# Kernel tuning notes

Measured on AMD Instinct MI355X. Metric: run time of the kernel, lower is better.

The kernel has to match this reference:

```python
import jax, jax.numpy as jnp
import numpy as np

LN_EPS = 1e-5
RMS_EPS = 1.1920929e-07  # torch RMSNorm default eps=None -> finfo(fp32).eps

B, N, D = 16, 512, 512
H = 8
HD = D // H
U_EMBED = 6
DFF = 4 * D


def _layernorm(x, w, b):
    mu = jnp.mean(x, axis=-1, keepdims=True)
    var = jnp.mean((x - mu) ** 2, axis=-1, keepdims=True)
    return (x - mu) * jax.lax.rsqrt(var + LN_EPS) * w + b


def _rmsnorm(x, w):
    ms = jnp.mean(x * x, axis=-1, keepdims=True)
    return x * jax.lax.rsqrt(ms + RMS_EPS) * w


def setup_inputs() -> dict:
    key = jax.random.key(0)
    ks = jax.random.split(key, 16)
    s = 0.02
    return {
        "x": jax.random.normal(ks[0], (B, N, D), jnp.float32),
        "u": jax.random.normal(ks[1], (B, U_EMBED, N, N), jnp.float32),
        "ln1_w": jnp.ones((D,), jnp.float32),
        "ln1_b": jnp.zeros((D,), jnp.float32),
        "ln2_w": jnp.ones((D,), jnp.float32),
        "ln2_b": jnp.zeros((D,), jnp.float32),
        "wq": jax.random.normal(ks[2], (D, D), jnp.float32) * s,
        "wk": jax.random.normal(ks[3], (D, D), jnp.float32) * s,
        "wv": jax.random.normal(ks[4], (D, D), jnp.float32) * s,
        "wo": jax.random.normal(ks[5], (D, D), jnp.float32) * s,
        "bo": jnp.zeros((D,), jnp.float32),
        "u_w": jax.random.normal(ks[6], (H, U_EMBED), jnp.float32) * 0.1,  # 1x1 conv kernel
        "u_b": jnp.zeros((H,), jnp.float32),
        "rms_w": jnp.ones((D,), jnp.float32),
        "w1": jax.random.normal(ks[7], (DFF, D), jnp.float32) * s,
        "b1": jnp.zeros((DFF,), jnp.float32),
        "w2": jax.random.normal(ks[8], (D, DFF), jnp.float32) * s,
        "b2": jnp.zeros((D,), jnp.float32),
    }


def reference(x, u, ln1_w, ln1_b, ln2_w, ln2_b, wq, wk, wv, wo, bo,
              u_w, u_b, rms_w, w1, b1, w2, b2):
    x_res = x
    xn = _layernorm(x, ln1_w, ln1_b)

    # projections -> [B, H, N, HD]
    q = jnp.einsum("bnd,ed->bne", xn, wq).reshape(B, N, H, HD).transpose(0, 2, 1, 3)
    k = jnp.einsum("bnd,ed->bne", xn, wk).reshape(B, N, H, HD).transpose(0, 2, 1, 3)
    v = jnp.einsum("bnd,ed->bne", xn, wv).reshape(B, N, H, HD).transpose(0, 2, 1, 3)

    # NOTE: source divides by head_dim**-0.5 (i.e. multiplies by sqrt(head_dim))
    scores = jnp.einsum("bhnd,bhmd->bhnm", q, k) * jnp.sqrt(jnp.float32(HD))

    # 1x1 conv pairwise bias: [B, u_embed, N, N] -> [B, H, N, N]
    u_bias = jnp.einsum("bcnm,hc->bhnm", u, u_w) + u_b[None, :, None, None]
    scores = scores + u_bias

    attn_weights = jax.nn.softmax(scores, axis=-1)
    ctx = jnp.einsum("bhnm,bhmd->bhnd", attn_weights, v)
    ctx = ctx.transpose(0, 2, 1, 3).reshape(B, N, D)
    attn_out = jnp.einsum("bnd,ed->bne", ctx, wo) + bo

    h = _layernorm(attn_out, ln2_w, ln2_b) + x_res

    z = _rmsnorm(h, rms_w)
    z = jax.nn.silu(jnp.einsum("bnd,fd->bnf", z, w1) + b1)
    z = jnp.einsum("bnf,df->bnd", z, w2) + b2
    return (z + h, attn_weights)
```

## Files before the change

kernel.cpp:

```cpp
#include <hip/hip_runtime.h>
#include <math.h>

static constexpr int Bb  = 16;
static constexpr int Nn  = 512;
static constexpr int Dd  = 512;
static constexpr int Hh  = 8;
static constexpr int HDd = 64;
static constexpr int UEe = 6;
static constexpr int DFFf= 2048;

typedef __attribute__((ext_vector_type(8))) short short8v;
typedef __attribute__((ext_vector_type(4))) float f32x4;

__device__ __forceinline__ short f2bf(float f) {
  unsigned u = __float_as_uint(f);
  unsigned r = (u + 0x7fffu + ((u >> 16) & 1u)) >> 16;
  return (short)r;
}
__device__ __forceinline__ float bf2f(short h) {
  return __uint_as_float(((unsigned)(unsigned short)h) << 16);
}
__device__ __forceinline__ void split2(float v, short& hi, short& lo) {
  hi = f2bf(v);
  lo = f2bf(v - bf2f(hi));
}


__device__ __forceinline__ float2 block_sum2(float a, float b, float* sb) {
  #pragma unroll
  for (int o = 32; o; o >>= 1) { a += __shfl_down(a, o); b += __shfl_down(b, o); }
  const int lane = threadIdx.x & 63, wid = threadIdx.x >> 6;
  if (lane == 0) { sb[wid] = a; sb[4 + wid] = b; }
  __syncthreads();
  float ra = sb[0] + sb[1] + sb[2] + sb[3];
  float rb = sb[4] + sb[5] + sb[6] + sb[7];
  __syncthreads();
  return make_float2(ra, rb);
}

__device__ __forceinline__ float block_sum1(float a, float* sb) {
  #pragma unroll
  for (int o = 32; o; o >>= 1) a += __shfl_down(a, o);
  const int lane = threadIdx.x & 63, wid = threadIdx.x >> 6;
  if (lane == 0) sb[wid] = a;
  __syncthreads();
  float ra = sb[0] + sb[1] + sb[2] + sb[3];
  __syncthreads();
  return ra;
}


__global__ __launch_bounds__(256) void ln1_kernel(
    const float* __restrict__ x, const float* __restrict__ w,
    const float* __restrict__ b, short* __restrict__ oh, short* __restrict__ ol) {
  __shared__ float sb[8];
  const size_t row = blockIdx.x;
  const int t = threadIdx.x;
  const float* xr = x + row * Dd;
  float2 xv = *(const float2*)(xr + 2 * t);
  float2 r = block_sum2(xv.x + xv.y, xv.x * xv.x + xv.y * xv.y, sb);
  const float mu = r.x * (1.f / Dd);
  const float var = r.y * (1.f / Dd) - mu * mu;
  const float rstd = rsqrtf(var + 1e-5f);
  float2 wv = *(const float2*)(w + 2 * t);
  float2 bv = *(const float2*)(b + 2 * t);
  float v0 = (xv.x - mu) * rstd * wv.x + bv.x;
  float v1 = (xv.y - mu) * rstd * wv.y + bv.y;
  short2 h2, l2;
  split2(v0, h2.x, l2.x);
  split2(v1, h2.y, l2.y);
  *(short2*)(oh + row * Dd + 2 * t) = h2;
  *(short2*)(ol + row * Dd + 2 * t) = l2;
}


__global__ __launch_bounds__(256) void hz_kernel(
    const float* __restrict__ ao, const float* __restrict__ xres,
    const float* __restrict__ w, const float* __restrict__ b,
    const float* __restrict__ rw,
    float* __restrict__ h, short* __restrict__ zbf) {
  __shared__ float sb[8];
  const size_t row = blockIdx.x;
  const int t = threadIdx.x;
  float2 av = *(const float2*)(ao + row * Dd + 2 * t);
  float2 r = block_sum2(av.x + av.y, av.x * av.x + av.y * av.y, sb);
  const float mu = r.x * (1.f / Dd);
  const float var = r.y * (1.f / Dd) - mu * mu;
  const float rstd = rsqrtf(var + 1e-5f);
  float2 wv = *(const float2*)(w + 2 * t);
  float2 bv = *(const float2*)(b + 2 * t);
  float2 xv = *(const float2*)(xres + row * Dd + 2 * t);
  float2 hv;
  hv.x = (av.x - mu) * rstd * wv.x + bv.x + xv.x;
  hv.y = (av.y - mu) * rstd * wv.y + bv.y + xv.y;
  *(float2*)(h + row * Dd + 2 * t) = hv;
  float ms = block_sum1(hv.x * hv.x + hv.y * hv.y, sb) * (1.f / Dd);
  const float rr = rsqrtf(ms + 1.1920929e-07f);
  float2 rwv = *(const float2*)(rw + 2 * t);
  short2 zv;
  zv.x = f2bf(hv.x * rr * rwv.x);
  zv.y = f2bf(hv.y * rr * rwv.y);
  *(short2*)(zbf + row * Dd + 2 * t) = zv;
}


__global__ __launch_bounds__(256) void cvt_kernel(
    const float* __restrict__ in, short* __restrict__ out, int n4) {
  int i = blockIdx.x * 256 + threadIdx.x;
  if (i < n4) {
    float4 v = ((const float4*)in)[i];
    short4 o;
    o.x = f2bf(v.x); o.y = f2bf(v.y); o.z = f2bf(v.z); o.w = f2bf(v.w);
    ((short4*)out)[i] = o;
  }
}

__global__ __launch_bounds__(256) void cvt2_kernel(
    const float* __restrict__ in, short* __restrict__ hi,
    short* __restrict__ lo, int n4) {
  int i = blockIdx.x * 256 + threadIdx.x;
  if (i < n4) {
    float4 v = ((const float4*)in)[i];
    short4 h, l;
    split2(v.x, h.x, l.x); split2(v.y, h.y, l.y);
    split2(v.z, h.z, l.z); split2(v.w, h.w, l.w);
    ((short4*)hi)[i] = h;
    ((short4*)lo)[i] = l;
  }
}


__global__ __launch_bounds__(256) void vt_kernel(
    const short* __restrict__ v, short* __restrict__ vT) {
  __shared__ short Lt[64][72];
  const int z = blockIdx.y, b = z >> 3, hh = z & 7;
  const int n0 = blockIdx.x * 64;
  const int tid = threadIdx.x;
  #pragma unroll
  for (int it = 0; it < 2; ++it) {
    int id = tid + it * 256;
    int r = id >> 3, c8 = id & 7;
    *(short8v*)&Lt[r][c8 * 8] =
        *(const short8v*)(v + ((size_t)(b * Nn + n0 + r)) * Dd + hh * HDd + c8 * 8);
  }
  __syncthreads();
  #pragma unroll
  for (int it = 0; it < 2; ++it) {
    int id = tid + it * 256;
    int c = id >> 3, r8 = id & 7;
    short8v g;
    #pragma unroll
    for (int k = 0; k < 8; ++k) g[k] = Lt[r8 * 8 + k][c];
    *(short8v*)(vT + ((size_t)z * HDd + c) * Nn + n0 + r8 * 8) = g;
  }
}


__global__ __launch_bounds__(256) void mfma_qkv3_kernel(
    const short* __restrict__ Ah, const short* __restrict__ Al,
    const short* __restrict__ Wh, const short* __restrict__ Wl,
    short* __restrict__ qh_, short* __restrict__ ql_,
    short* __restrict__ kh_, short* __restrict__ kl_,
    short* __restrict__ vh_) {
  constexpr int MREP = 4, NREP = 2;
  __shared__ short Ash[128][40], Asl[128][40], Bsh[64][40], Bsl[64][40];
  const int tid = threadIdx.x;
  const int wave = tid >> 6, lane = tid & 63;
  const int wr = wave >> 1, wc = wave & 1;
  const int lrow = lane & 15, kblk = lane >> 4;
  const size_t bm = (size_t)blockIdx.y * 128, bn = (size_t)blockIdx.x * 64;
  f32x4 acc[MREP][NREP] = {};
  for (int k0 = 0; k0 < Dd; k0 += 32) {
    __syncthreads();
    #pragma unroll
    for (int it = 0; it < 2; ++it) {
      int id = tid + it * 256;
      int r = id >> 2, kq = id & 3;
      const size_t go = (bm + r) * Dd + k0 + kq * 8;
      *(short8v*)&Ash[r][kq * 8] = *(const short8v*)(Ah + go);
      *(short8v*)&Asl[r][kq * 8] = *(const short8v*)(Al + go);
    }
    {
      int r = tid >> 2, kq = tid & 3;
      const size_t go = (bn + r) * Dd + k0 + kq * 8;
      *(short8v*)&Bsh[r][kq * 8] = *(const short8v*)(Wh + go);
      *(short8v*)&Bsl[r][kq * 8] = *(const short8v*)(Wl + go);
    }
    __syncthreads();
    short8v afh[MREP], afl[MREP], bfh[NREP], bfl[NREP];
    #pragma unroll
    for (int i = 0; i < MREP; ++i) {
      afh[i] = *(const short8v*)&Ash[wr * 64 + i * 16 + lrow][kblk * 8];
      afl[i] = *(const short8v*)&Asl[wr * 64 + i * 16 + lrow][kblk * 8];
    }
    #pragma unroll
    for (int j = 0; j < NREP; ++j) {
      bfh[j] = *(const short8v*)&Bsh[wc * 32 + j * 16 + lrow][kblk * 8];
      bfl[j] = *(const short8v*)&Bsl[wc * 32 + j * 16 + lrow][kblk * 8];
    }
    #pragma unroll
    for (int i = 0; i < MREP; ++i)
      #pragma unroll
      for (int j = 0; j < NREP; ++j) {
        acc[i][j] = __builtin_amdgcn_mfma_f32_16x16x32_bf16(afh[i], bfh[j], acc[i][j], 0, 0, 0);
        acc[i][j] = __builtin_amdgcn_mfma_f32_16x16x32_bf16(afl[i], bfh[j], acc[i][j], 0, 0, 0);
        acc[i][j] = __builtin_amdgcn_mfma_f32_16x16x32_bf16(afh[i], bfl[j], acc[i][j], 0, 0, 0);
      }
  }
  const int seg = (int)(bn >> 9);
  short* dsth = seg == 0 ? qh_ : (seg == 1 ? kh_ : vh_);
  short* dstl = seg == 0 ? ql_ : kl_;
  #pragma unroll
  for (int i = 0; i < MREP; ++i) {
    #pragma unroll
    for (int j = 0; j < NREP; ++j) {
      const size_t gcol = (bn & 511) + wc * 32 + j * 16 + lrow;
      #pragma unroll
      for (int reg = 0; reg < 4; ++reg) {
        const size_t grow = bm + wr * 64 + i * 16 + kblk * 4 + reg;
        float vv = acc[i][j][reg];
        if (seg < 2) {
          short hh_, ll_;
          split2(vv, hh_, ll_);
          dsth[grow * Dd + gcol] = hh_;
          dstl[grow * Dd + gcol] = ll_;
        } else {
          dsth[grow * Dd + gcol] = f2bf(vv);
        }
      }
    }
  }
}


template <int EPI>
__global__ __launch_bounds__(256) void mfma_nt3_kernel(
    const short* __restrict__ Ah, const short* __restrict__ Al,
    const short* __restrict__ Wh, const short* __restrict__ Wl,
    void* __restrict__ C1, void* __restrict__ C2,
    const float* __restrict__ bias, int Nc, int K) {
  constexpr int BM = 128, BN = 64;
  constexpr int MREP = 4, NREP = 2;
  __shared__ short Ash[BM][40], Asl[BM][40], Bsh[BN][40], Bsl[BN][40];
  const int tid = threadIdx.x;
  const int wave = tid >> 6, lane = tid & 63;
  const int wr = wave >> 1, wc = wave & 1;
  const int lrow = lane & 15, kblk = lane >> 4;
  const size_t bm = (size_t)blockIdx.y * BM, bn = (size_t)blockIdx.x * BN;
  f32x4 acc[MREP][NREP] = {};
  for (int k0 = 0; k0 < K; k0 += 32) {
    __syncthreads();
    #pragma unroll
    for (int it = 0; it < 2; ++it) {
      int id = tid + it * 256;
      int r = id >> 2, kq = id & 3;
      const size_t go = (bm + r) * K + k0 + kq * 8;
      *(short8v*)&Ash[r][kq * 8] = *(const short8v*)(Ah + go);
      *(short8v*)&Asl[r][kq * 8] = *(const short8v*)(Al + go);
    }
    {
      int r = tid >> 2, kq = tid & 3;
      const size_t go = (bn + r) * K + k0 + kq * 8;
      *(short8v*)&Bsh[r][kq * 8] = *(const short8v*)(Wh + go);
      *(short8v*)&Bsl[r][kq * 8] = *(const short8v*)(Wl + go);
    }
    __syncthreads();
    short8v afh[MREP], afl[MREP], bfh[NREP], bfl[NREP];
    #pragma unroll
    for (int i = 0; i < MREP; ++i) {
      afh[i] = *(const short8v*)&Ash[wr * 64 + i * 16 + lrow][kblk * 8];
      afl[i] = *(const short8v*)&Asl[wr * 64 + i * 16 + lrow][kblk * 8];
    }
    #pragma unroll
    for (int j = 0; j < NREP; ++j) {
      bfh[j] = *(const short8v*)&Bsh[wc * 32 + j * 16 + lrow][kblk * 8];
      bfl[j] = *(const short8v*)&Bsl[wc * 32 + j * 16 + lrow][kblk * 8];
    }
    #pragma unroll
    for (int i = 0; i < MREP; ++i)
      #pragma unroll
      for (int j = 0; j < NREP; ++j) {
        acc[i][j] = __builtin_amdgcn_mfma_f32_16x16x32_bf16(afh[i], bfh[j], acc[i][j], 0, 0, 0);
        acc[i][j] = __builtin_amdgcn_mfma_f32_16x16x32_bf16(afl[i], bfh[j], acc[i][j], 0, 0, 0);
        acc[i][j] = __builtin_amdgcn_mfma_f32_16x16x32_bf16(afh[i], bfl[j], acc[i][j], 0, 0, 0);
      }
  }
  #pragma unroll
  for (int i = 0; i < MREP; ++i) {
    #pragma unroll
    for (int j = 0; j < NREP; ++j) {
      const size_t gcol = bn + wc * 32 + j * 16 + lrow;
      float bb = 0.f;
      if constexpr (EPI == 1) bb = bias[gcol];
      #pragma unroll
      for (int reg = 0; reg < 4; ++reg) {
        const size_t grow = bm + wr * 64 + i * 16 + kblk * 4 + reg;
        float vv = acc[i][j][reg] + bb;
        if constexpr (EPI == 0) {
          short hh_, ll_;
          split2(vv, hh_, ll_);
          ((short*)C1)[grow * Nc + gcol] = hh_;
          ((short*)C2)[grow * Nc + gcol] = ll_;
        } else if constexpr (EPI == 1) {
          ((float*)C1)[grow * Nc + gcol] = vv;
        } else {
          ((short*)C1)[grow * Nc + gcol] = f2bf(vv);
        }
      }
    }
  }
}


__global__ __launch_bounds__(256) void scores8_kernel(
    const short* __restrict__ qh, const short* __restrict__ ql,
    const short* __restrict__ kh, const short* __restrict__ kl,
    float* __restrict__ S, const float* __restrict__ u,
    const float* __restrict__ u_w, const float* __restrict__ u_b) {
  __shared__ __align__(16) char smem[36864];
  short (*Qsh)[72] = (short(*)[72])(smem + 0);
  short (*Qsl)[72] = (short(*)[72])(smem + 9216);
  short (*Ksh)[72] = (short(*)[72])(smem + 18432);
  short (*Ksl)[72] = (short(*)[72])(smem + 27648);
  float (*Sls)[68] = (float(*)[68])(smem);
  const int b = blockIdx.z;
  const int i0 = blockIdx.y * 64, j0 = blockIdx.x * 64;
  const int tid = threadIdx.x;
  const int wave = tid >> 6, lane = tid & 63;
  const int wr = wave >> 1, wc = wave & 1;
  const int lrow = lane & 15, kblk = lane >> 4;
  const int trow = tid >> 4;
  const int tcol = (tid & 15) * 4;
  const float* ub_ = u + (size_t)b * UEe * Nn * Nn;

  for (int h = 0; h < Hh; ++h) {
    __syncthreads();
    #pragma unroll
    for (int it = 0; it < 2; ++it) {
      int id = tid + it * 256;
      int r = id >> 3, kq = id & 7;
      const size_t gq = ((size_t)(b * Nn) + i0 + r) * Dd + h * HDd + kq * 8;
      const size_t gk = ((size_t)(b * Nn) + j0 + r) * Dd + h * HDd + kq * 8;
      *(short8v*)&Qsh[r][kq * 8] = *(const short8v*)(qh + gq);
      *(short8v*)&Qsl[r][kq * 8] = *(const short8v*)(ql + gq);
      *(short8v*)&Ksh[r][kq * 8] = *(const short8v*)(kh + gk);
      *(short8v*)&Ksl[r][kq * 8] = *(const short8v*)(kl + gk);
    }
    __syncthreads();
    f32x4 acc[2][2] = {};
    #pragma unroll
    for (int ks = 0; ks < 2; ++ks) {
      short8v afh[2], afl[2], bfh[2], bfl[2];
      #pragma unroll
      for (int i = 0; i < 2; ++i) {
        afh[i] = *(const short8v*)&Qsh[wr * 32 + i * 16 + lrow][ks * 32 + kblk * 8];
        afl[i] = *(const short8v*)&Qsl[wr * 32 + i * 16 + lrow][ks * 32 + kblk * 8];
      }
      #pragma unroll
      for (int j = 0; j < 2; ++j) {
        bfh[j] = *(const short8v*)&Ksh[wc * 32 + j * 16 + lrow][ks * 32 + kblk * 8];
        bfl[j] = *(const short8v*)&Ksl[wc * 32 + j * 16 + lrow][ks * 32 + kblk * 8];
      }
      #pragma unroll
      for (int i = 0; i < 2; ++i)
        #pragma unroll
        for (int j = 0; j < 2; ++j) {
          acc[i][j] = __builtin_amdgcn_mfma_f32_16x16x32_bf16(afh[i], bfh[j], acc[i][j], 0, 0, 0);
          acc[i][j] = __builtin_amdgcn_mfma_f32_16x16x32_bf16(afl[i], bfh[j], acc[i][j], 0, 0, 0);
          acc[i][j] = __builtin_amdgcn_mfma_f32_16x16x32_bf16(afh[i], bfl[j], acc[i][j], 0, 0, 0);
        }
    }
    __syncthreads();
    #pragma unroll
    for (int i = 0; i < 2; ++i)
      #pragma unroll
      for (int j = 0; j < 2; ++j)
        #pragma unroll
        for (int reg = 0; reg < 4; ++reg)
          Sls[wr * 32 + i * 16 + kblk * 4 + reg][wc * 32 + j * 16 + lrow] =
              8.f * acc[i][j][reg];
    __syncthreads();
    float uw[UEe];
    #pragma unroll
    for (int c = 0; c < UEe; ++c) uw[c] = u_w[h * UEe + c];
    const float ubh = u_b[h];
    float* Sp = S + ((size_t)(b * Hh + h)) * Nn * Nn;
    #pragma unroll
    for (int p = 0; p < 4; ++p) {
      const size_t goff = (size_t)(i0 + p * 16 + trow) * Nn + j0 + tcol;
      float4 v = *(const float4*)&Sls[p * 16 + trow][tcol];
      v.x += ubh; v.y += ubh; v.z += ubh; v.w += ubh;
      #pragma unroll
      for (int c = 0; c < UEe; ++c) {
        float4 uv = *(const float4*)(ub_ + (size_t)c * Nn * Nn + goff);
        v.x = fmaf(uw[c], uv.x, v.x);
        v.y = fmaf(uw[c], uv.y, v.y);
        v.z = fmaf(uw[c], uv.z, v.z);
        v.w = fmaf(uw[c], uv.w, v.w);
      }
      *(float4*)(Sp + goff) = v;
    }
  }
}


__global__ __launch_bounds__(256) void smctx_kernel(
    float* __restrict__ P, const short* __restrict__ vT,
    short* __restrict__ ctxh, short* __restrict__ ctxl) {
  __shared__ short Ps[32][520];
  __shared__ short Bs[64][136];
  const int z = blockIdx.y, b = z >> 3, hh = z & 7;
  const int row0 = blockIdx.x * 32;
  const int tid = threadIdx.x;
  const int lr = tid >> 3, sub = tid & 7;
  float* Sp = P + (size_t)z * Nn * Nn + (size_t)(row0 + lr) * Nn + sub * 64;
  float4 s[16];
  #pragma unroll
  for (int q = 0; q < 16; ++q) s[q] = *(const float4*)(Sp + q * 4);
  float m = -1e30f;
  #pragma unroll
  for (int q = 0; q < 16; ++q)
    m = fmaxf(m, fmaxf(fmaxf(s[q].x, s[q].y), fmaxf(s[q].z, s[q].w)));
  m = fmaxf(m, __shfl_xor(m, 1));
  m = fmaxf(m, __shfl_xor(m, 2));
  m = fmaxf(m, __shfl_xor(m, 4));
  float sum = 0.f;
  #pragma unroll
  for (int q = 0; q < 16; ++q) {
    s[q].x = __expf(s[q].x - m); s[q].y = __expf(s[q].y - m);
    s[q].z = __expf(s[q].z - m); s[q].w = __expf(s[q].w - m);
    sum += (s[q].x + s[q].y) + (s[q].z + s[q].w);
  }
  sum += __shfl_xor(sum, 1);
  sum += __shfl_xor(sum, 2);
  sum += __shfl_xor(sum, 4);
  const float rr = 1.f / sum;
  #pragma unroll
  for (int q = 0; q < 16; ++q) {
    s[q].x *= rr; s[q].y *= rr; s[q].z *= rr; s[q].w *= rr;
    *(float4*)(Sp + q * 4) = s[q];
  }
  #pragma unroll
  for (int q = 0; q < 8; ++q) {
    float4 a = s[2 * q], c = s[2 * q + 1];
    short8v pk;
    pk[0] = f2bf(a.x); pk[1] = f2bf(a.y); pk[2] = f2bf(a.z); pk[3] = f2bf(a.w);
    pk[4] = f2bf(c.x); pk[5] = f2bf(c.y); pk[6] = f2bf(c.z); pk[7] = f2bf(c.w);
    *(short8v*)&Ps[lr][sub * 64 + q * 8] = pk;
  }
  const int wave = tid >> 6, lane = tid & 63;
  const int wr = wave >> 1, wc = wave & 1;
  const int lrow = lane & 15, kblk = lane >> 4;
  f32x4 acc0 = {}, acc1 = {};
  for (int kc = 0; kc < 4; ++kc) {
    __syncthreads();
    #pragma unroll
    for (int it = 0; it < 4; ++it) {
      int id = tid + it * 256;
      int rrow = id >> 4, k8 = id & 15;
      *(short8v*)&Bs[rrow][k8 * 8] =
          *(const short8v*)(vT + ((size_t)z * HDd + rrow) * Nn + kc * 128 + k8 * 8);
    }
    __syncthreads();
    #pragma unroll
    for (int ks = 0; ks < 4; ++ks) {
      short8v af = *(const short8v*)&Ps[wr * 16 + lrow][kc * 128 + ks * 32 + kblk * 8];
      short8v b0 = *(const short8v*)&Bs[wc * 32 + lrow][ks * 32 + kblk * 8];
      short8v b1 = *(const short8v*)&Bs[wc * 32 + 16 + lrow][ks * 32 + kblk * 8];
      acc0 = __builtin_amdgcn_mfma_f32_16x16x32_bf16(af, b0, acc0, 0, 0, 0);
      acc1 = __builtin_amdgcn_mfma_f32_16x16x32_bf16(af, b1, acc1, 0, 0, 0);
    }
  }
  const size_t outbase =
      ((size_t)(b * Nn + row0 + wr * 16 + kblk * 4)) * Dd + hh * HDd + wc * 32 + lrow;
  #pragma unroll
  for (int reg = 0; reg < 4; ++reg) {
    short h0, l0, h1, l1;
    split2(acc0[reg], h0, l0);
    split2(acc1[reg], h1, l1);
    ctxh[outbase + (size_t)reg * Dd] = h0;
    ctxl[outbase + (size_t)reg * Dd] = l0;
    ctxh[outbase + (size_t)reg * Dd + 16] = h1;
    ctxl[outbase + (size_t)reg * Dd + 16] = l1;
  }
}


template <int BM, int BN, int EPI>
__global__ __launch_bounds__(256) void mfma_nt_kernel(
    const short* __restrict__ Ag, const short* __restrict__ Wg,
    void* __restrict__ Cv, const float* __restrict__ bias,
    const float* __restrict__ res, int Nc, int K) {
  constexpr int MREP = BM / 32, NREP = BN / 32;
  __shared__ short As[BM][72];
  __shared__ short Bs[BN][72];
  const int tid = threadIdx.x;
  const int wave = tid >> 6, lane = tid & 63;
  const int wr = wave >> 1, wc = wave & 1;
  const int lrow = lane & 15, kblk = lane >> 4;
  const size_t bm = (size_t)blockIdx.y * BM, bn = (size_t)blockIdx.x * BN;
  f32x4 acc[MREP][NREP] = {};
  for (int k0 = 0; k0 < K; k0 += 32) {
    __syncthreads();
    #pragma unroll
    for (int it = 0; it < BM / 64; ++it) {
      int id = tid + it * 256;
      int r = id >> 2, kq = id & 3;
      *(short8v*)&As[r][kq * 8] = *(const short8v*)(Ag + (bm + r) * K + k0 + kq * 8);
    }
    #pragma unroll
    for (int it = 0; it < BN / 64; ++it) {
      int id = tid + it * 256;
      int r = id >> 2, kq = id & 3;
      *(short8v*)&Bs[r][kq * 8] = *(const short8v*)(Wg + (bn + r) * K + k0 + kq * 8);
    }
    __syncthreads();
    short8v af[MREP], bf[NREP];
    #pragma unroll
    for (int i = 0; i < MREP; ++i)
      af[i] = *(const short8v*)&As[wr * (BM / 2) + i * 16 + lrow][kblk * 8];
    #pragma unroll
    for (int j = 0; j < NREP; ++j)
      bf[j] = *(const short8v*)&Bs[wc * (BN / 2) + j * 16 + lrow][kblk * 8];
    #pragma unroll
    for (int i = 0; i < MREP; ++i)
      #pragma unroll
      for (int j = 0; j < NREP; ++j)
        acc[i][j] = __builtin_amdgcn_mfma_f32_16x16x32_bf16(af[i], bf[j], acc[i][j], 0, 0, 0);
  }
  #pragma unroll
  for (int i = 0; i < MREP; ++i) {
    #pragma unroll
    for (int j = 0; j < NREP; ++j) {
      const size_t gcol = bn + wc * (BN / 2) + j * 16 + lrow;
      const float bb = bias[gcol];
      #pragma unroll
      for (int reg = 0; reg < 4; ++reg) {
        const size_t grow = bm + wr * (BM / 2) + i * 16 + kblk * 4 + reg;
        float vv = acc[i][j][reg] + bb;
        if constexpr (EPI == 0) {
          vv = vv / (1.f + __expf(-vv));
          ((short*)Cv)[grow * Nc + gcol] = f2bf(vv);
        } else {
          ((float*)Cv)[grow * Nc + gcol] = vv + res[grow * Nc + gcol];
        }
      }
    }
  }
}


extern "C" void kernel_launch(void* const* d_in, const int* in_sizes, int n_in,
                              void* d_out, int out_size, void* d_ws, size_t ws_size,
                              hipStream_t stream) {
  const float* x     = (const float*)d_in[0];
  const float* u     = (const float*)d_in[1];
  const float* ln1_w = (const float*)d_in[2];
  const float* ln1_b = (const float*)d_in[3];
  const float* ln2_w = (const float*)d_in[4];
  const float* ln2_b = (const float*)d_in[5];
  const float* wq    = (const float*)d_in[6];
  const float* wk    = (const float*)d_in[7];
  const float* wv    = (const float*)d_in[8];
  const float* wo    = (const float*)d_in[9];
  const float* bo    = (const float*)d_in[10];
  const float* u_w   = (const float*)d_in[11];
  const float* u_b   = (const float*)d_in[12];
  const float* rms_w = (const float*)d_in[13];
  const float* w1    = (const float*)d_in[14];
  const float* b1    = (const float*)d_in[15];
  const float* w2    = (const float*)d_in[16];
  const float* b2    = (const float*)d_in[17];

  float* out   = (float*)d_out;
  float* attnW = out + (size_t)Bb * Nn * Dd;

  const size_t SB = (size_t)Bb * Nn * Dd * 2;
  char* wsb = (char*)d_ws;
  short* xnh  = (short*)(wsb + 0 * SB);
  short* xnl  = (short*)(wsb + 1 * SB);
  short* qh   = (short*)(wsb + 2 * SB);
  short* ql   = (short*)(wsb + 3 * SB);
  short* kh   = (short*)(wsb + 4 * SB);
  short* kl   = (short*)(wsb + 5 * SB);
  short* vh   = (short*)(wsb + 6 * SB);
  short* vTh  = (short*)(wsb + 0 * SB);
  short* ctxh = (short*)(wsb + 1 * SB);
  short* ctxl = (short*)(wsb + 6 * SB);
  float* aout = (float*)(wsb + 2 * SB);
  float* hbuf = (float*)(wsb + 5 * SB);
  short* zbf  = (short*)(wsb + 0 * SB);
  short* h1bf = (short*)(wsb + 1 * SB);
  const size_t WTBYTES = 8 * (size_t)Dd * Dd * 2 + 2 * (size_t)DFFf * Dd * 2;
  const size_t wt = (ws_size - WTBYTES) & ~(size_t)255;
  short* wAh = (short*)(wsb + wt);
  short* wAl = wAh + 3 * (size_t)Dd * Dd;
  short* woh = wAl + 3 * (size_t)Dd * Dd;
  short* wol = woh + (size_t)Dd * Dd;
  short* w1h = wol + (size_t)Dd * Dd;
  short* w2h = w1h + (size_t)DFFf * Dd;

  const int MR = Bb * Nn;

  cvt2_kernel<<<256, 256, 0, stream>>>(wq, wAh, wAl, Dd * Dd / 4);
  cvt2_kernel<<<256, 256, 0, stream>>>(wk, wAh + (size_t)Dd * Dd, wAl + (size_t)Dd * Dd, Dd * Dd / 4);
  cvt2_kernel<<<256, 256, 0, stream>>>(wv, wAh + 2 * (size_t)Dd * Dd, wAl + 2 * (size_t)Dd * Dd, Dd * Dd / 4);
  cvt2_kernel<<<256, 256, 0, stream>>>(wo, woh, wol, Dd * Dd / 4);
  cvt_kernel<<<1024, 256, 0, stream>>>(w1, w1h, DFFf * Dd / 4);
  cvt_kernel<<<1024, 256, 0, stream>>>(w2, w2h, DFFf * Dd / 4);

  ln1_kernel<<<MR, 256, 0, stream>>>(x, ln1_w, ln1_b, xnh, xnl);

  dim3 gQKV(3 * Dd / 64, MR / 128);
  mfma_qkv3_kernel<<<gQKV,256,0,stream>>>(xnh, xnl, wAh, wAl, qh, ql, kh, kl, vh);

  dim3 gVt(Nn / 64, Bb * Hh);
  vt_kernel<<<gVt, 256, 0, stream>>>(vh, vTh);

  dim3 gSc(Nn / 64, Nn / 64, Bb);
  scores8_kernel<<<gSc, 256, 0, stream>>>(qh, ql, kh, kl, attnW, u, u_w, u_b);

  dim3 gSm(Nn / 32, Bb * Hh);
  smctx_kernel<<<gSm, 256, 0, stream>>>(attnW, vTh, ctxh, ctxl);

  dim3 gProj(Dd / 64, MR / 128);
  mfma_nt3_kernel<1><<<gProj,256,0,stream>>>(ctxh, ctxl, woh, wol, aout, nullptr, bo, Dd, Dd);

  hz_kernel<<<MR, 256, 0, stream>>>(aout, x, ln2_w, ln2_b, rms_w, hbuf, zbf);

  dim3 gF1(DFFf / 128, MR / 128);
  mfma_nt_kernel<128,128,0><<<gF1,256,0,stream>>>(
      zbf, w1h, h1bf, b1, nullptr, DFFf, Dd);
  dim3 gF2(Dd / 128, MR / 64);
  mfma_nt_kernel<64,128,1><<<gF2,256,0,stream>>>(
      h1bf, w2h, out, b2, hbuf, Dd, DFFf);
}
```

Measured before the change: 346.2 us.

## Fuse scores, pairwise bias, softmax and context into one attention kernel

Merges the scores kernel (QK^T plus 1x1-conv bias) and the softmax+PV kernel into a single kernel per (batch, head, 32-row block). Scores for a row block stay in registers, so the fp32 score matrix is written once as the final attention weights instead of being written, read back and rewritten. In exchange, the u bias tensor is now read once per head instead of once per batch across all heads, K is reloaded per 32-row block, and shared memory per block grows.

```diff
diff --git a/kernel.cpp b/kernel.cpp
--- a/kernel.cpp
+++ b/kernel.cpp
@@ -312,83 +312,78 @@
 }
 
 
-__global__ __launch_bounds__(256) void scores8_kernel(
+__global__ __launch_bounds__(256) void fattn_kernel(
     const short* __restrict__ qh, const short* __restrict__ ql,
     const short* __restrict__ kh, const short* __restrict__ kl,
-    float* __restrict__ S, const float* __restrict__ u,
-    const float* __restrict__ u_w, const float* __restrict__ u_b) {
-  __shared__ __align__(16) char smem[36864];
+    const short* __restrict__ vT, float* __restrict__ P,
+    const float* __restrict__ u, const float* __restrict__ u_w,
+    const float* __restrict__ u_b,
+    short* __restrict__ ctxh, short* __restrict__ ctxl) {
+  __shared__ __align__(16) char smem[50688];
   short (*Qsh)[72] = (short(*)[72])(smem + 0);
-  short (*Qsl)[72] = (short(*)[72])(smem + 9216);
-  short (*Ksh)[72] = (short(*)[72])(smem + 18432);
-  short (*Ksl)[72] = (short(*)[72])(smem + 27648);
-  float (*Sls)[68] = (float(*)[68])(smem);
-  const int b = blockIdx.z;
-  const int i0 = blockIdx.y * 64, j0 = blockIdx.x * 64;
+  short (*Qsl)[72] = (short(*)[72])(smem + 4608);
+  short (*Ksh)[72] = (short(*)[72])(smem + 9216);
+  short (*Ksl)[72] = (short(*)[72])(smem + 18432);
+  float (*Sls)[68] = (float(*)[68])(smem + 27648);
+  short (*Ps)[520] = (short(*)[520])(smem + 0);
+  short (*Bs)[136] = (short(*)[136])(smem + 33280);
+  const int z = blockIdx.y, b = z >> 3, h = z & 7;
+  const int row0 = blockIdx.x * 32;
   const int tid = threadIdx.x;
+  const int lr = tid >> 3, sub = tid & 7;
   const int wave = tid >> 6, lane = tid & 63;
   const int wr = wave >> 1, wc = wave & 1;
   const int lrow = lane & 15, kblk = lane >> 4;
-  const int trow = tid >> 4;
-  const int tcol = (tid & 15) * 4;
+
+  {
+    const size_t gq = ((size_t)(b * Nn) + row0 + lr) * Dd + h * HDd + sub * 8;
+    *(short8v*)&Qsh[lr][sub * 8] = *(const short8v*)(qh + gq);
+    *(short8v*)&Qsl[lr][sub * 8] = *(const short8v*)(ql + gq);
+  }
+  float uw[UEe];
+  #pragma unroll
+  for (int c = 0; c < UEe; ++c) uw[c] = u_w[h * UEe + c];
+  const float ubh = u_b[h];
   const float* ub_ = u + (size_t)b * UEe * Nn * Nn;
 
-  for (int h = 0; h < Hh; ++h) {
+  float4 s[16];
+  #pragma unroll
+  for (int jt = 0; jt < 8; ++jt) {
     __syncthreads();
     #pragma unroll
     for (int it = 0; it < 2; ++it) {
       int id = tid + it * 256;
       int r = id >> 3, kq = id & 7;
-      const size_t gq = ((size_t)(b * Nn) + i0 + r) * Dd + h * HDd + kq * 8;
-      const size_t gk = ((size_t)(b * Nn) + j0 + r) * Dd + h * HDd + kq * 8;
-      *(short8v*)&Qsh[r][kq * 8] = *(const short8v*)(qh + gq);
-      *(short8v*)&Qsl[r][kq * 8] = *(const short8v*)(ql + gq);
+      const size_t gk = ((size_t)(b * Nn) + jt * 64 + r) * Dd + h * HDd + kq * 8;
       *(short8v*)&Ksh[r][kq * 8] = *(const short8v*)(kh + gk);
       *(short8v*)&Ksl[r][kq * 8] = *(const short8v*)(kl + gk);
     }
     __syncthreads();
-    f32x4 acc[2][2] = {};
+    f32x4 acc[2] = {};
     #pragma unroll
     for (int ks = 0; ks < 2; ++ks) {
-      short8v afh[2], afl[2], bfh[2], bfl[2];
-      #pragma unroll
-      for (int i = 0; i < 2; ++i) {
-        afh[i] = *(const short8v*)&Qsh[wr * 32 + i * 16 + lrow][ks * 32 + kblk * 8];
-        afl[i] = *(const short8v*)&Qsl[wr * 32 + i * 16 + lrow][ks * 32 + kblk * 8];
+      short8v afh = *(const short8v*)&Qsh[wr * 16 + lrow][ks * 32 + kblk * 8];
+      short8v afl = *(const short8v*)&Qsl[wr * 16 + lrow][ks * 32 + kblk * 8];
+      #pragma unroll
+      for (int j = 0; j < 2; ++j) {
+        short8v bfh = *(const short8v*)&Ksh[wc * 32 + j * 16 + lrow][ks * 32 + kblk * 8];
+        short8v bfl = *(const short8v*)&Ksl[wc * 32 + j * 16 + lrow][ks * 32 + kblk * 8];
+        acc[j] = __builtin_amdgcn_mfma_f32_16x16x32_bf16(afh, bfh, acc[j], 0, 0, 0);
+        acc[j] = __builtin_amdgcn_mfma_f32_16x16x32_bf16(afl, bfh, acc[j], 0, 0, 0);
+        acc[j] = __builtin_amdgcn_mfma_f32_16x16x32_bf16(afh, bfl, acc[j], 0, 0, 0);
       }
-      #pragma unroll
-      for (int j = 0; j < 2; ++j) {
-        bfh[j] = *(const short8v*)&Ksh[wc * 32 + j * 16 + lrow][ks * 32 + kblk * 8];
-        bfl[j] = *(const short8v*)&Ksl[wc * 32 + j * 16 + lrow][ks * 32 + kblk * 8];
-      }
-      #pragma unroll
-      for (int i = 0; i < 2; ++i)
-        #pragma unroll
-        for (int j = 0; j < 2; ++j) {
-          acc[i][j] = __builtin_amdgcn_mfma_f32_16x16x32_bf16(afh[i], bfh[j], acc[i][j], 0, 0, 0);
-          acc[i][j] = __builtin_amdgcn_mfma_f32_16x16x32_bf16(afl[i], bfh[j], acc[i][j], 0, 0, 0);
-          acc[i][j] = __builtin_amdgcn_mfma_f32_16x16x32_bf16(afh[i], bfl[j], acc[i][j], 0, 0, 0);
-        }
-    }
-    __syncthreads();
-    #pragma unroll
-    for (int i = 0; i < 2; ++i)
-      #pragma unroll
-      for (int j = 0; j < 2; ++j)
-        #pragma unroll
-        for (int reg = 0; reg < 4; ++reg)
-          Sls[wr * 32 + i * 16 + kblk * 4 + reg][wc * 32 + j * 16 + lrow] =
-              8.f * acc[i][j][reg];
-    __syncthreads();
-    float uw[UEe];
-    #pragma unroll
-    for (int c = 0; c < UEe; ++c) uw[c] = u_w[h * UEe + c];
-    const float ubh = u_b[h];
-    float* Sp = S + ((size_t)(b * Hh + h)) * Nn * Nn;
-    #pragma unroll
-    for (int p = 0; p < 4; ++p) {
-      const size_t goff = (size_t)(i0 + p * 16 + trow) * Nn + j0 + tcol;
-      float4 v = *(const float4*)&Sls[p * 16 + trow][tcol];
+    }
+    #pragma unroll
+    for (int j = 0; j < 2; ++j)
+      #pragma unroll
+      for (int reg = 0; reg < 4; ++reg)
+        Sls[wr * 16 + kblk * 4 + reg][wc * 32 + j * 16 + lrow] = 8.f * acc[j][reg];
+    __syncthreads();
+    #pragma unroll
+    for (int dt = 0; dt < 2; ++dt) {
+      const int t = jt * 2 + dt;
+      float4 v = *(const float4*)&Sls[lr][dt * 32 + sub * 4];
+      const size_t goff = (size_t)(row0 + lr) * Nn + 4 * (sub + 8 * t);
       v.x += ubh; v.y += ubh; v.z += ubh; v.w += ubh;
       #pragma unroll
       for (int c = 0; c < UEe; ++c) {
@@ -398,25 +393,11 @@
         v.z = fmaf(uw[c], uv.z, v.z);
         v.w = fmaf(uw[c], uv.w, v.w);
       }
-      *(float4*)(Sp + goff) = v;
-    }
-  }
-}
-
-
-__global__ __launch_bounds__(256) void smctx_kernel(
-    float* __restrict__ P, const short* __restrict__ vT,
-    short* __restrict__ ctxh, short* __restrict__ ctxl) {
-  __shared__ short Ps[32][520];
-  __shared__ short Bs[64][136];
-  const int z = blockIdx.y, b = z >> 3, hh = z & 7;
-  const int row0 = blockIdx.x * 32;
-  const int tid = threadIdx.x;
-  const int lr = tid >> 3, sub = tid & 7;
-  float* Sp = P + (size_t)z * Nn * Nn + (size_t)(row0 + lr) * Nn + sub * 64;
-  float4 s[16];
-  #pragma unroll
-  for (int q = 0; q < 16; ++q) s[q] = *(const float4*)(Sp + q * 4);
+      s[t] = v;
+    }
+  }
+  __syncthreads();
+
   float m = -1e30f;
   #pragma unroll
   for (int q = 0; q < 16; ++q)
@@ -435,22 +416,17 @@
   sum += __shfl_xor(sum, 2);
   sum += __shfl_xor(sum, 4);
   const float rr = 1.f / sum;
+  float* Pp = P + (size_t)z * Nn * Nn + (size_t)(row0 + lr) * Nn;
   #pragma unroll
   for (int q = 0; q < 16; ++q) {
     s[q].x *= rr; s[q].y *= rr; s[q].z *= rr; s[q].w *= rr;
-    *(float4*)(Sp + q * 4) = s[q];
-  }
-  #pragma unroll
-  for (int q = 0; q < 8; ++q) {
-    float4 a = s[2 * q], c = s[2 * q + 1];
-    short8v pk;
-    pk[0] = f2bf(a.x); pk[1] = f2bf(a.y); pk[2] = f2bf(a.z); pk[3] = f2bf(a.w);
-    pk[4] = f2bf(c.x); pk[5] = f2bf(c.y); pk[6] = f2bf(c.z); pk[7] = f2bf(c.w);
-    *(short8v*)&Ps[lr][sub * 64 + q * 8] = pk;
-  }
-  const int wave = tid >> 6, lane = tid & 63;
-  const int wr = wave >> 1, wc = wave & 1;
-  const int lrow = lane & 15, kblk = lane >> 4;
+    const int col = 4 * (sub + 8 * q);
+    *(float4*)(Pp + col) = s[q];
+    short4 pk;
+    pk.x = f2bf(s[q].x); pk.y = f2bf(s[q].y);
+    pk.z = f2bf(s[q].z); pk.w = f2bf(s[q].w);
+    *(short4*)&Ps[lr][col] = pk;
+  }
   f32x4 acc0 = {}, acc1 = {};
   for (int kc = 0; kc < 4; ++kc) {
     __syncthreads();
@@ -472,7 +448,7 @@
     }
   }
   const size_t outbase =
-      ((size_t)(b * Nn + row0 + wr * 16 + kblk * 4)) * Dd + hh * HDd + wc * 32 + lrow;
+      ((size_t)(b * Nn + row0 + wr * 16 + kblk * 4)) * Dd + h * HDd + wc * 32 + lrow;
   #pragma unroll
   for (int reg = 0; reg < 4; ++reg) {
     short h0, l0, h1, l1;
@@ -617,11 +593,9 @@
   dim3 gVt(Nn / 64, Bb * Hh);
   vt_kernel<<<gVt, 256, 0, stream>>>(vh, vTh);
 
-  dim3 gSc(Nn / 64, Nn / 64, Bb);
-  scores8_kernel<<<gSc, 256, 0, stream>>>(qh, ql, kh, kl, attnW, u, u_w, u_b);
-
-  dim3 gSm(Nn / 32, Bb * Hh);
-  smctx_kernel<<<gSm, 256, 0, stream>>>(attnW, vTh, ctxh, ctxl);
+  dim3 gFa(Nn / 32, Bb * Hh);
+  fattn_kernel<<<gFa, 256, 0, stream>>>(qh, ql, kh, kl, vTh, attnW,
+                                        u, u_w, u_b, ctxh, ctxl);
 
   dim3 gProj(Dd / 64, MR / 128);
   mfma_nt3_kernel<1><<<gProj,256,0,stream>>>(ctxh, ctxl, woh, wol, aout, nullptr, bo, Dd, Dd);
```

New measurement: 348.2 us. About the same (+0.6%).
